# Kernel tuning notes

Measured on AMD Instinct MI355X. Metric: run time of the kernel, lower is better.

The kernel has to match this reference:

```python
import jax, jax.numpy as jnp
import numpy as np
import math

B, S, D_IN, D_Q = 4, 2048, 512, 512

def setup_inputs() -> dict:
    key = jax.random.key(0)
    ks = jax.random.split(key, 7)
    s_in = 1.0 / math.sqrt(D_IN)
    x = jax.random.normal(ks[0], (B, S, D_IN), dtype=jnp.float32)
    # nn.Linear-style params: W [out,in], b [out]; uniform(-1/sqrt(in), 1/sqrt(in))
    Wq = jax.random.uniform(ks[1], (D_Q, D_IN), jnp.float32, -s_in, s_in)
    bq = jax.random.uniform(ks[2], (D_Q,), jnp.float32, -s_in, s_in)
    Wk = jax.random.uniform(ks[3], (D_Q, D_IN), jnp.float32, -s_in, s_in)
    bk = jax.random.uniform(ks[4], (D_Q,), jnp.float32, -s_in, s_in)
    Wv = jax.random.uniform(ks[5], (D_Q, D_IN), jnp.float32, -s_in, s_in)
    bv = jax.random.uniform(ks[6], (D_Q,), jnp.float32, -s_in, s_in)
    return {"x": x, "Wq": Wq, "bq": bq, "Wk": Wk, "bk": bk, "Wv": Wv, "bv": bv}

def reference(x, Wq, bq, Wk, bk, Wv, bv):
    # Q/K/V projections: [B,S,D_IN] @ W^T + b -> [B,S,D_Q]
    Q = jnp.einsum('bsi,qi->bsq', x, Wq) + bq
    K = jnp.einsum('bsi,qi->bsq', x, Wk) + bk
    V = jnp.einsum('bsi,qi->bsq', x, Wv) + bv
    scale = 1.0 / math.sqrt(D_Q)
    scores = jnp.einsum('bsq,btq->bst', Q, K) * scale  # [B,S,S]
    attention = jax.nn.softmax(scores, axis=-1)        # 'atten_prob'
    weighted = jnp.einsum('bst,btq->bsq', attention, V)  # 'atten_score'
    return (attention, weighted)
```

## Files before the change

kernel.cpp:

```cpp
#include <hip/hip_runtime.h>
#include <hip/hip_bf16.h>

typedef unsigned short u16;
typedef short bf16x8 __attribute__((ext_vector_type(8)));
typedef float f32x4 __attribute__((ext_vector_type(4)));

#define S_LEN 2048
#define DQ 512
#define NBATCH 4

__device__ __forceinline__ u16 f2bf(float f) {
    __hip_bfloat16 h = __float2bfloat16(f);
    return *reinterpret_cast<u16*>(&h);
}
__device__ __forceinline__ float bf2f(u16 u) {
    unsigned v = ((unsigned)u) << 16;
    union { unsigned u; float f; } c; c.u = v; return c.f;
}

__device__ __forceinline__ void async16(const u16* g, u16* l) {
    __builtin_amdgcn_global_load_lds(
        (__attribute__((address_space(1))) void*)g,
        (__attribute__((address_space(3))) void*)l, 16, 0, 0);
}

__device__ __forceinline__ int xcd_swz(int bid, int chunk) {
    return (bid & 7) * chunk + (bid >> 3);
}

__global__ __launch_bounds__(256) void k_cvt_all(const float* __restrict__ x,
                                                 const float* __restrict__ wq,
                                                 const float* __restrict__ wk,
                                                 const float* __restrict__ wv,
                                                 u16* __restrict__ xb, u16* __restrict__ wb,
                                                 float* __restrict__ sums) {
    int bid = blockIdx.x;
    if (bid >= 4864) {
        int i = (bid - 4864) * 256 + threadIdx.x;
        *(f32x4*)(sums + (size_t)i * 4) = (f32x4)0.0f;
        return;
    }
    const float* src;
    u16* dst;
    int i;
    if (bid < 4096)      { src = x;  dst = xb;          i = bid * 256 + threadIdx.x; }
    else if (bid < 4352) { src = wq; dst = wb;          i = (bid - 4096) * 256 + threadIdx.x; }
    else if (bid < 4608) { src = wk; dst = wb + 262144; i = (bid - 4352) * 256 + threadIdx.x; }
    else                 { src = wv; dst = wb + 524288; i = (bid - 4608) * 256 + threadIdx.x; }
    f32x4 v = *(const f32x4*)(src + (size_t)i * 4);
    ushort4 o;
    o.x = f2bf(v.x); o.y = f2bf(v.y); o.z = f2bf(v.z); o.w = f2bf(v.w);
    *(ushort4*)(dst + (size_t)i * 4) = o;
}

__device__ __forceinline__ void stage_unit(const u16* __restrict__ G, u16* buf,
                                           int kcol, int h, int tid) {
#pragma unroll
    for (int q = 0; q < 2; ++q) {
        int c   = q * 512 + tid;
        int r   = c >> 3;
        int p   = c & 7;
        int lch = p ^ (r & 7);
        async16(G + (size_t)(h * 128 + r) * DQ + kcol + lch * 8,
                buf + h * 8192 + c * 8);
    }
}

__device__ __forceinline__ void gemm256(const u16* __restrict__ A, const u16* __restrict__ B,
                                        u16* ldsA, u16* ldsB, f32x4 acc[8][4], int tid) {
    const int lane = tid & 63;
    const int w    = tid >> 6;
    const int wr   = w >> 2;
    const int wc   = w & 3;
    const int l16  = lane & 15;
    const int quad = lane >> 4;
    const int p0   = quad ^ (l16 & 7);
    const int a0   = (wr * 128 + l16) * 64 + p0 * 8;
    const int a1   = (wr * 128 + l16) * 64 + (p0 ^ 4) * 8;
    const int b0   = (wc * 64 + l16) * 64 + p0 * 8;
    const int b1   = (wc * 64 + l16) * 64 + (p0 ^ 4) * 8;

    stage_unit(A, ldsA, 0, 0, tid);
    stage_unit(A, ldsA, 0, 1, tid);
    stage_unit(B, ldsB, 0, 0, tid);
    stage_unit(B, ldsB, 0, 1, tid);
    __syncthreads();

    for (int kt = 0; kt < 8; ++kt) {
        const u16* rdA = ldsA + (kt & 1) * 16384;
        const u16* rdB = ldsB + (kt & 1) * 16384;
        u16* wrA = ldsA + ((kt + 1) & 1) * 16384;
        u16* wrB = ldsB + ((kt + 1) & 1) * 16384;
        const int  kc = (kt + 1) * 64;
        const bool pf = kt < 7;
        bf16x8 a[4][2], bbf[2][2];

        if (pf) stage_unit(A, wrA, kc, 0, tid);
#pragma unroll
        for (int i = 0; i < 4; ++i) {
            a[i][0] = *(const bf16x8*)(rdA + a0 + i * 1024);
            a[i][1] = *(const bf16x8*)(rdA + a1 + i * 1024);
        }
#pragma unroll
        for (int j = 0; j < 2; ++j) {
            bbf[j][0] = *(const bf16x8*)(rdB + b0 + j * 1024);
            bbf[j][1] = *(const bf16x8*)(rdB + b1 + j * 1024);
        }
        __builtin_amdgcn_s_setprio(1);
#pragma unroll
        for (int i = 0; i < 4; ++i)
#pragma unroll
            for (int j = 0; j < 2; ++j) {
                acc[i][j] = __builtin_amdgcn_mfma_f32_16x16x32_bf16(a[i][0], bbf[j][0], acc[i][j], 0, 0, 0);
                acc[i][j] = __builtin_amdgcn_mfma_f32_16x16x32_bf16(a[i][1], bbf[j][1], acc[i][j], 0, 0, 0);
            }
        __builtin_amdgcn_s_setprio(0);

        if (pf) stage_unit(A, wrA, kc, 1, tid);
#pragma unroll
        for (int j = 0; j < 2; ++j) {
            bbf[j][0] = *(const bf16x8*)(rdB + b0 + (2 + j) * 1024);
            bbf[j][1] = *(const bf16x8*)(rdB + b1 + (2 + j) * 1024);
        }
        __builtin_amdgcn_s_setprio(1);
#pragma unroll
        for (int i = 0; i < 4; ++i)
#pragma unroll
            for (int j = 0; j < 2; ++j) {
                acc[i][2 + j] = __builtin_amdgcn_mfma_f32_16x16x32_bf16(a[i][0], bbf[j][0], acc[i][2 + j], 0, 0, 0);
                acc[i][2 + j] = __builtin_amdgcn_mfma_f32_16x16x32_bf16(a[i][1], bbf[j][1], acc[i][2 + j], 0, 0, 0);
            }
        __builtin_amdgcn_s_setprio(0);

        if (pf) stage_unit(B, wrB, kc, 0, tid);
#pragma unroll
        for (int i = 0; i < 4; ++i) {
            a[i][0] = *(const bf16x8*)(rdA + a0 + (4 + i) * 1024);
            a[i][1] = *(const bf16x8*)(rdA + a1 + (4 + i) * 1024);
        }
        __builtin_amdgcn_s_setprio(1);
#pragma unroll
        for (int i = 0; i < 4; ++i)
#pragma unroll
            for (int j = 0; j < 2; ++j) {
                acc[4 + i][2 + j] = __builtin_amdgcn_mfma_f32_16x16x32_bf16(a[i][0], bbf[j][0], acc[4 + i][2 + j], 0, 0, 0);
                acc[4 + i][2 + j] = __builtin_amdgcn_mfma_f32_16x16x32_bf16(a[i][1], bbf[j][1], acc[4 + i][2 + j], 0, 0, 0);
            }
        __builtin_amdgcn_s_setprio(0);

        if (pf) stage_unit(B, wrB, kc, 1, tid);
#pragma unroll
        for (int j = 0; j < 2; ++j) {
            bbf[j][0] = *(const bf16x8*)(rdB + b0 + j * 1024);
            bbf[j][1] = *(const bf16x8*)(rdB + b1 + j * 1024);
        }
        __builtin_amdgcn_s_setprio(1);
#pragma unroll
        for (int i = 0; i < 4; ++i)
#pragma unroll
            for (int j = 0; j < 2; ++j) {
                acc[4 + i][j] = __builtin_amdgcn_mfma_f32_16x16x32_bf16(a[i][0], bbf[j][0], acc[4 + i][j], 0, 0, 0);
                acc[4 + i][j] = __builtin_amdgcn_mfma_f32_16x16x32_bf16(a[i][1], bbf[j][1], acc[4 + i][j], 0, 0, 0);
            }
        __builtin_amdgcn_s_setprio(0);

        __syncthreads();
    }
}

__global__ __launch_bounds__(512, 2) void k_proj(const u16* __restrict__ xb, const u16* __restrict__ Wb,
                                                 const float* __restrict__ bq, const float* __restrict__ bk,
                                                 const float* __restrict__ bv, u16* __restrict__ out,
                                                 u16* __restrict__ VT) {
    __shared__ __align__(16) u16 lds[65536];
    const int l  = xcd_swz(blockIdx.x, 24);
    const int bx = l & 1;
    const int by = (l >> 1) & 31;
    const int z  = l >> 6;
    const int m0 = by * 256, n0 = bx * 256;
    const u16* A = xb + (size_t)m0 * DQ;
    const u16* B = Wb + (size_t)z * DQ * DQ + (size_t)n0 * DQ;
    const float* bias = (z == 0) ? bq : (z == 1) ? bk : bv;

    f32x4 acc[8][4];
#pragma unroll
    for (int i = 0; i < 8; ++i)
#pragma unroll
        for (int j = 0; j < 4; ++j) acc[i][j] = (f32x4)0.0f;

    const int tid = threadIdx.x;
    gemm256(A, B, lds, lds + 32768, acc, tid);

    const int lane = tid & 63, w = tid >> 6;
    const int wr = w >> 2, wc = w & 3;
    const int l16 = lane & 15, quad = lane >> 4;

    if (z < 2) {
        u16* outz = out + (size_t)z * 8192 * DQ;
#pragma unroll
        for (int j = 0; j < 4; ++j) {
            int gn = n0 + wc * 64 + j * 16 + l16;
            float bv_ = bias[gn];
#pragma unroll
            for (int i = 0; i < 8; ++i)
#pragma unroll
                for (int r = 0; r < 4; ++r) {
                    int gm = m0 + wr * 128 + i * 16 + quad * 4 + r;
                    outz[(size_t)gm * DQ + gn] = f2bf(acc[i][j][r] + bv_);
                }
        }
    } else {
        const int bb_ = m0 >> 11;
        u16* VTb_ = VT + (size_t)bb_ * DQ * S_LEN;
#pragma unroll
        for (int j = 0; j < 4; ++j) {
            int gn = n0 + wc * 64 + j * 16 + l16;
            float bv_ = bias[gn];
#pragma unroll
            for (int i = 0; i < 8; ++i) {
                int t0 = (m0 & 2047) + wr * 128 + i * 16 + quad * 4;
                ushort4 o;
                o.x = f2bf(acc[i][j][0] + bv_);
                o.y = f2bf(acc[i][j][1] + bv_);
                o.z = f2bf(acc[i][j][2] + bv_);
                o.w = f2bf(acc[i][j][3] + bv_);
                *(ushort4*)(VTb_ + (size_t)gn * S_LEN + t0) = o;
            }
        }
    }
}

__global__ __launch_bounds__(512, 2) void k_scores(const u16* __restrict__ Qb, const u16* __restrict__ Kb,
                                                   u16* __restrict__ Pb, float* __restrict__ sums) {
    __shared__ __align__(16) u16 lds[65536];
    const int l  = xcd_swz(blockIdx.x, 32);
    const int bx = l & 7;
    const int by = (l >> 3) & 7;
    const int b  = l >> 6;
    const int m0 = by * 256, n0 = bx * 256;
    const u16* A = Qb + ((size_t)b * S_LEN + m0) * DQ;
    const u16* B = Kb + ((size_t)b * S_LEN + n0) * DQ;

    f32x4 acc[8][4];
#pragma unroll
    for (int i = 0; i < 8; ++i)
#pragma unroll
        for (int j = 0; j < 4; ++j) acc[i][j] = (f32x4)0.0f;

    const int tid = threadIdx.x;
    gemm256(A, B, lds, lds + 32768, acc, tid);

    const float scale = 0.044194173824159216f;
    const int lane = tid & 63, w = tid >> 6;
    const int wr = w >> 2, wc = w & 3;
    const int l16 = lane & 15, quad = lane >> 4;
    u16* prow = Pb + (size_t)(b * S_LEN + m0) * S_LEN;

    float psum[8][4];
#pragma unroll
    for (int i = 0; i < 8; ++i)
#pragma unroll
        for (int r = 0; r < 4; ++r) psum[i][r] = 0.0f;

#pragma unroll
    for (int i = 0; i < 8; ++i)
#pragma unroll
        for (int j = 0; j < 4; ++j)
#pragma unroll
            for (int r = 0; r < 4; ++r) {
                int gm = wr * 128 + i * 16 + quad * 4 + r;
                int gn = n0 + wc * 64 + j * 16 + l16;
                float e = __expf(acc[i][j][r] * scale);
                u16 pbv = f2bf(e);
                prow[(size_t)gm * S_LEN + gn] = pbv;
                psum[i][r] += bf2f(pbv);
            }

    float* sums_row = sums + b * S_LEN + m0 + wr * 128;
#pragma unroll
    for (int i = 0; i < 8; ++i)
#pragma unroll
        for (int r = 0; r < 4; ++r) {
            float v = psum[i][r];
            v += __shfl_xor(v, 1);
            v += __shfl_xor(v, 2);
            v += __shfl_xor(v, 4);
            v += __shfl_xor(v, 8);
            if (l16 == 0) atomicAdd(&sums_row[i * 16 + quad * 4 + r], v);
        }
}

__global__ __launch_bounds__(256) void k_pv(const u16* __restrict__ Pb, const u16* __restrict__ VT,
                                            const float* __restrict__ sums,
                                            float* __restrict__ probs,
                                            float* __restrict__ wout) {
    __shared__ __align__(16) u16 lds[12288];
    u16* ldsA = lds;
    u16* ldsB = lds + 8192;
    const int l  = xcd_swz(blockIdx.x, 64);
    const int bx = l & 7;
    const int by = (l >> 3) & 15;
    const int b  = l >> 7;
    const int m0 = by * 128, n0 = bx * 64;
    const u16* A = Pb + (size_t)(b * S_LEN + m0) * S_LEN;
    const u16* B = VT + (size_t)b * DQ * S_LEN + (size_t)n0 * S_LEN;

    const int tid  = threadIdx.x;
    const int lane = tid & 63;
    const int w    = tid >> 6;
    const int wm   = (w & 1) << 6;
    const int wn   = (w >> 1) << 5;
    const int l16  = lane & 15;
    const int quad = lane >> 4;

    f32x4 acc[4][2];
#pragma unroll
    for (int i = 0; i < 4; ++i)
#pragma unroll
        for (int j = 0; j < 2; ++j) acc[i][j] = (f32x4)0.0f;

    for (int k0 = 0; k0 < S_LEN; k0 += 64) {
#pragma unroll
        for (int h = 0; h < 2; ++h) {
#pragma unroll
            for (int it = 0; it < 2; ++it) {
                int c  = it * 256 + tid;
                int r  = c >> 2;
                int cc = (c & 3) << 3;
                async16(A + (size_t)r * S_LEN + k0 + h * 32 + cc, ldsA + h * 4096 + r * 32 + cc);
            }
            {
                int r  = tid >> 2;
                int cc = (tid & 3) << 3;
                async16(B + (size_t)r * S_LEN + k0 + h * 32 + cc, ldsB + h * 2048 + r * 32 + cc);
            }
        }
        __syncthreads();
        bf16x8 af[2][4], bfr[2][2];
#pragma unroll
        for (int h = 0; h < 2; ++h) {
#pragma unroll
            for (int i = 0; i < 4; ++i)
                af[h][i] = *(const bf16x8*)(ldsA + h * 4096 + (wm + i * 16 + l16) * 32 + quad * 8);
#pragma unroll
            for (int j = 0; j < 2; ++j)
                bfr[h][j] = *(const bf16x8*)(ldsB + h * 2048 + (wn + j * 16 + l16) * 32 + quad * 8);
        }
#pragma unroll
        for (int h = 0; h < 2; ++h)
#pragma unroll
            for (int i = 0; i < 4; ++i)
#pragma unroll
                for (int j = 0; j < 2; ++j)
                    acc[i][j] = __builtin_amdgcn_mfma_f32_16x16x32_bf16(af[h][i], bfr[h][j], acc[i][j], 0, 0, 0);
        __syncthreads();
    }

    float* ldsInv = (float*)lds;
    if (tid < 128) ldsInv[tid] = 1.0f / sums[b * S_LEN + m0 + tid];
    __syncthreads();

    float* outb = wout + (size_t)b * S_LEN * DQ;
#pragma unroll
    for (int i = 0; i < 4; ++i) {
#pragma unroll
        for (int r = 0; r < 4; ++r) {
            int lm = wm + i * 16 + quad * 4 + r;
            float inv = ldsInv[lm];
#pragma unroll
            for (int j = 0; j < 2; ++j) {
                int gn = n0 + wn + j * 16 + l16;
                outb[(size_t)(m0 + lm) * DQ + gn] = acc[i][j][r] * inv;
            }
        }
    }

    const u16* Psl = Pb + (size_t)(b * S_LEN + m0) * S_LEN + bx * 256;
    float* Pro = probs + ((size_t)b * S_LEN + m0) * S_LEN + bx * 256;
#pragma unroll
    for (int it = 0; it < 16; ++it) {
        int idx = it * 256 + tid;
        int r  = idx >> 5;
        int cc = (idx & 31) << 3;
        float inv = ldsInv[r];
        bf16x8 vv = *(const bf16x8*)(Psl + (size_t)r * S_LEN + cc);
        f32x4 o0, o1;
        o0.x = bf2f((u16)vv[0]) * inv;
        o0.y = bf2f((u16)vv[1]) * inv;
        o0.z = bf2f((u16)vv[2]) * inv;
        o0.w = bf2f((u16)vv[3]) * inv;
        o1.x = bf2f((u16)vv[4]) * inv;
        o1.y = bf2f((u16)vv[5]) * inv;
        o1.z = bf2f((u16)vv[6]) * inv;
        o1.w = bf2f((u16)vv[7]) * inv;
        float* dst = Pro + (size_t)r * S_LEN + cc;
        *(f32x4*)(dst) = o0;
        *(f32x4*)(dst + 4) = o1;
    }
}

extern "C" void kernel_launch(void* const* d_in, const int* in_sizes, int n_in,
                              void* d_out, int out_size, void* d_ws, size_t ws_size,
                              hipStream_t stream) {
    const float* x  = (const float*)d_in[0];
    const float* Wq = (const float*)d_in[1];
    const float* bq = (const float*)d_in[2];
    const float* Wk = (const float*)d_in[3];
    const float* bk = (const float*)d_in[4];
    const float* Wv = (const float*)d_in[5];
    const float* bv = (const float*)d_in[6];

    char* ws = (char*)d_ws;
    u16* xb  = (u16*)(ws);
    u16* Wb  = (u16*)(ws + 8388608);
    u16* Qb  = (u16*)(ws + 9961472);
    u16* Kb  = (u16*)(ws + 18350080);
    u16* VTb = (u16*)(ws + 35127296);
    u16* Pb  = (u16*)(ws + 43515904);
    float* sums = (float*)(ws + 77070336);
    float* probs = (float*)d_out;
    float* wout  = (float*)d_out + 16777216;

    k_cvt_all<<<4872, 256, 0, stream>>>(x, Wq, Wk, Wv, xb, Wb, sums);
    k_proj<<<192, 512, 0, stream>>>(xb, Wb, bq, bk, bv, Qb, VTb);
    k_scores<<<256, 512, 0, stream>>>(Qb, Kb, Pb, sums);
    k_pv<<<512, 256, 0, stream>>>(Pb, VTb, sums, probs, wout);
}
```

Before: 193.0 us.

## Double-buffer P·V kernel with swizzled LDS and larger 128x128 tiles

Restructures the P·V GEMM kernel to 512-thread blocks computing 128x128 output tiles, halving the number of times the P matrix is streamed from memory. Adds double-buffered LDS with prefetch of the next K tile interleaved with MFMA compute, and XOR-swizzled LDS layout to avoid bank conflicts. Also uses s_setprio around MFMA bursts. Uses more LDS (64KB) per block which may limit occupancy.

Result: faster. 187.2 us (-3.0%).

```diff
diff --git a/kernel.cpp b/kernel.cpp
--- a/kernel.cpp
+++ b/kernel.cpp
@@ -290,28 +290,43 @@
         }
 }
 
-__global__ __launch_bounds__(256) void k_pv(const u16* __restrict__ Pb, const u16* __restrict__ VT,
-                                            const float* __restrict__ sums,
-                                            float* __restrict__ probs,
-                                            float* __restrict__ wout) {
-    __shared__ __align__(16) u16 lds[12288];
+__device__ __forceinline__ void stage_pv(const u16* __restrict__ G, u16* buf,
+                                         int kcol, int h, int tid) {
+    int c   = tid;
+    int r   = c >> 3;
+    int p   = c & 7;
+    int lch = p ^ (r & 7);
+    async16(G + (size_t)(h * 64 + r) * S_LEN + kcol + lch * 8,
+            buf + h * 4096 + c * 8);
+}
+
+__global__ __launch_bounds__(512, 2) void k_pv(const u16* __restrict__ Pb, const u16* __restrict__ VT,
+                                               const float* __restrict__ sums,
+                                               float* __restrict__ probs,
+                                               float* __restrict__ wout) {
+    __shared__ __align__(16) u16 lds[32768];
     u16* ldsA = lds;
-    u16* ldsB = lds + 8192;
-    const int l  = xcd_swz(blockIdx.x, 64);
-    const int bx = l & 7;
-    const int by = (l >> 3) & 15;
-    const int b  = l >> 7;
-    const int m0 = by * 128, n0 = bx * 64;
+    u16* ldsB = lds + 16384;
+    const int l  = xcd_swz(blockIdx.x, 32);
+    const int bx = l & 3;
+    const int by = (l >> 2) & 15;
+    const int b  = l >> 6;
+    const int m0 = by * 128, n0 = bx * 128;
     const u16* A = Pb + (size_t)(b * S_LEN + m0) * S_LEN;
     const u16* B = VT + (size_t)b * DQ * S_LEN + (size_t)n0 * S_LEN;
 
     const int tid  = threadIdx.x;
     const int lane = tid & 63;
     const int w    = tid >> 6;
-    const int wm   = (w & 1) << 6;
-    const int wn   = (w >> 1) << 5;
+    const int wr   = w >> 2;
+    const int wc   = w & 3;
     const int l16  = lane & 15;
     const int quad = lane >> 4;
+    const int p0   = quad ^ (l16 & 7);
+    const int a0   = (wr * 64 + l16) * 64 + p0 * 8;
+    const int a1   = (wr * 64 + l16) * 64 + (p0 ^ 4) * 8;
+    const int b0   = (wc * 32 + l16) * 64 + p0 * 8;
+    const int b1   = (wc * 32 + l16) * 64 + (p0 ^ 4) * 8;
 
     f32x4 acc[4][2];
 #pragma unroll
@@ -319,40 +334,48 @@
 #pragma unroll
         for (int j = 0; j < 2; ++j) acc[i][j] = (f32x4)0.0f;
 
-    for (int k0 = 0; k0 < S_LEN; k0 += 64) {
-#pragma unroll
-        for (int h = 0; h < 2; ++h) {
-#pragma unroll
-            for (int it = 0; it < 2; ++it) {
-                int c  = it * 256 + tid;
-                int r  = c >> 2;
-                int cc = (c & 3) << 3;
-                async16(A + (size_t)r * S_LEN + k0 + h * 32 + cc, ldsA + h * 4096 + r * 32 + cc);
-            }
-            {
-                int r  = tid >> 2;
-                int cc = (tid & 3) << 3;
-                async16(B + (size_t)r * S_LEN + k0 + h * 32 + cc, ldsB + h * 2048 + r * 32 + cc);
-            }
-        }
-        __syncthreads();
-        bf16x8 af[2][4], bfr[2][2];
-#pragma unroll
-        for (int h = 0; h < 2; ++h) {
-#pragma unroll
-            for (int i = 0; i < 4; ++i)
-                af[h][i] = *(const bf16x8*)(ldsA + h * 4096 + (wm + i * 16 + l16) * 32 + quad * 8);
-#pragma unroll
-            for (int j = 0; j < 2; ++j)
-                bfr[h][j] = *(const bf16x8*)(ldsB + h * 2048 + (wn + j * 16 + l16) * 32 + quad * 8);
-        }
-#pragma unroll
-        for (int h = 0; h < 2; ++h)
-#pragma unroll
-            for (int i = 0; i < 4; ++i)
-#pragma unroll
-                for (int j = 0; j < 2; ++j)
-                    acc[i][j] = __builtin_amdgcn_mfma_f32_16x16x32_bf16(af[h][i], bfr[h][j], acc[i][j], 0, 0, 0);
+    stage_pv(A, ldsA, 0, 0, tid);
+    stage_pv(A, ldsA, 0, 1, tid);
+    stage_pv(B, ldsB, 0, 0, tid);
+    stage_pv(B, ldsB, 0, 1, tid);
+    __syncthreads();
+
+    for (int kt = 0; kt < 32; ++kt) {
+        const u16* rdA = ldsA + (kt & 1) * 8192;
+        const u16* rdB = ldsB + (kt & 1) * 8192;
+        u16* wrA = ldsA + ((kt + 1) & 1) * 8192;
+        u16* wrB = ldsB + ((kt + 1) & 1) * 8192;
+        const int  kc = (kt + 1) * 64;
+        const bool pf = kt < 31;
+        bf16x8 a[4][2], bbf[2];
+
+        if (pf) { stage_pv(A, wrA, kc, 0, tid); stage_pv(A, wrA, kc, 1, tid); }
+#pragma unroll
+        for (int i = 0; i < 4; ++i) {
+            a[i][0] = *(const bf16x8*)(rdA + a0 + i * 1024);
+            a[i][1] = *(const bf16x8*)(rdA + a1 + i * 1024);
+        }
+        bbf[0] = *(const bf16x8*)(rdB + b0);
+        bbf[1] = *(const bf16x8*)(rdB + b1);
+        __builtin_amdgcn_s_setprio(1);
+#pragma unroll
+        for (int i = 0; i < 4; ++i) {
+            acc[i][0] = __builtin_amdgcn_mfma_f32_16x16x32_bf16(a[i][0], bbf[0], acc[i][0], 0, 0, 0);
+            acc[i][0] = __builtin_amdgcn_mfma_f32_16x16x32_bf16(a[i][1], bbf[1], acc[i][0], 0, 0, 0);
+        }
+        __builtin_amdgcn_s_setprio(0);
+
+        if (pf) { stage_pv(B, wrB, kc, 0, tid); stage_pv(B, wrB, kc, 1, tid); }
+        bbf[0] = *(const bf16x8*)(rdB + b0 + 1024);
+        bbf[1] = *(const bf16x8*)(rdB + b1 + 1024);
+        __builtin_amdgcn_s_setprio(1);
+#pragma unroll
+        for (int i = 0; i < 4; ++i) {
+            acc[i][1] = __builtin_amdgcn_mfma_f32_16x16x32_bf16(a[i][0], bbf[0], acc[i][1], 0, 0, 0);
+            acc[i][1] = __builtin_amdgcn_mfma_f32_16x16x32_bf16(a[i][1], bbf[1], acc[i][1], 0, 0, 0);
+        }
+        __builtin_amdgcn_s_setprio(0);
+
         __syncthreads();
     }
 
@@ -365,23 +388,23 @@
     for (int i = 0; i < 4; ++i) {
 #pragma unroll
         for (int r = 0; r < 4; ++r) {
-            int lm = wm + i * 16 + quad * 4 + r;
+            int lm = wr * 64 + i * 16 + quad * 4 + r;
             float inv = ldsInv[lm];
 #pragma unroll
             for (int j = 0; j < 2; ++j) {
-                int gn = n0 + wn + j * 16 + l16;
+                int gn = n0 + wc * 32 + j * 16 + l16;
                 outb[(size_t)(m0 + lm) * DQ + gn] = acc[i][j][r] * inv;
             }
         }
     }
 
-    const u16* Psl = Pb + (size_t)(b * S_LEN + m0) * S_LEN + bx * 256;
-    float* Pro = probs + ((size_t)b * S_LEN + m0) * S_LEN + bx * 256;
+    const u16* Psl = Pb + (size_t)(b * S_LEN + m0) * S_LEN + bx * 512;
+    float* Pro = probs + ((size_t)b * S_LEN + m0) * S_LEN + bx * 512;
 #pragma unroll
     for (int it = 0; it < 16; ++it) {
-        int idx = it * 256 + tid;
-        int r  = idx >> 5;
-        int cc = (idx & 31) << 3;
+        int idx = it * 512 + tid;
+        int r  = idx >> 6;
+        int cc = (idx & 63) << 3;
         float inv = ldsInv[r];
         bf16x8 vv = *(const bf16x8*)(Psl + (size_t)r * S_LEN + cc);
         f32x4 o0, o1;
@@ -424,5 +447,5 @@
     k_cvt_all<<<4872, 256, 0, stream>>>(x, Wq, Wk, Wv, xb, Wb, sums);
     k_proj<<<192, 512, 0, stream>>>(xb, Wb, bq, bk, bv, Qb, VTb);
     k_scores<<<256, 512, 0, stream>>>(Qb, Kb, Pb, sums);
-    k_pv<<<512, 256, 0, stream>>>(Pb, VTb, sums, probs, wout);
-}
+    k_pv<<<256, 512, 0, stream>>>(Pb, VTb, sums, probs, wout);
+}
```
